# Kernel tuning notes

Measured on AMD Instinct MI355X. Metric: run time of the kernel, lower is better.

## Reference

```python
import jax, jax.numpy as jnp
import numpy as np

NUM_NODES = 50000
NUM_EDGES = 400000
NUM_GRAPHS = 16


def _glorot(key, shape):
    fan_in, fan_out = shape[0], shape[1]
    lim = jnp.sqrt(6.0 / (fan_in + fan_out))
    return jax.random.uniform(key, shape, jnp.float32, -lim, lim)


def setup_inputs() -> dict:
    key = jax.random.key(0)
    ks = jax.random.split(key, 12)
    x = jax.random.normal(ks[0], (NUM_NODES, 3), jnp.float32)
    edge_index = jax.random.randint(ks[1], (2, NUM_EDGES), 0, NUM_NODES, jnp.int64)
    batch = jax.random.randint(ks[2], (NUM_NODES,), 0, NUM_GRAPHS, jnp.int64)
    return {
        "x": x,
        "edge_index": edge_index,
        "batch": batch,
        "W1": _glorot(ks[3], (3, 512)),   "b1": jnp.zeros((512,), jnp.float32),
        "W2": _glorot(ks[4], (512, 1024)), "b2": jnp.zeros((1024,), jnp.float32),
        "W3": _glorot(ks[5], (1024, 512)), "b3": jnp.zeros((512,), jnp.float32),
        "fcw1": _glorot(ks[6], (512, 128)), "fcb1": jnp.zeros((128,), jnp.float32),
        "fcw2": _glorot(ks[7], (128, 1)),   "fcb2": jnp.zeros((1,), jnp.float32),
    }


def _gcn_conv(x, W, b, row, col, n):
    # PyG GCNConv: h = x W; out_i = sum_{j->i} d_j^{-1/2} d_i^{-1/2} h_j + b
    # (row, col) already include self-loops; edge weights are 1.
    h = x @ W  # [N, out]
    deg = jnp.zeros((n,), h.dtype).at[col].add(1.0)  # in-degree incl. self-loop
    dis = jax.lax.rsqrt(deg)  # deg >= 1 thanks to self-loops
    norm = dis[row] * dis[col]  # [E]
    msgs = h[row] * norm[:, None]  # [E, out] gather
    return jax.ops.segment_sum(msgs, col, num_segments=n) + b


def reference(x, edge_index, batch, W1, b1, W2, b2, W3, b3, fcw1, fcb1, fcw2, fcb2):
    n = x.shape[0]
    loop = jnp.arange(n, dtype=edge_index.dtype)
    row = jnp.concatenate([edge_index[0], loop])  # source
    col = jnp.concatenate([edge_index[1], loop])  # target

    h = jax.nn.relu(_gcn_conv(x, W1, b1, row, col, n))
    h = jax.nn.relu(_gcn_conv(h, W2, b2, row, col, n))
    h = jax.nn.relu(_gcn_conv(h, W3, b3, row, col, n))

    # global mean pool over graphs in the batch
    sums = jax.ops.segment_sum(h, batch, num_segments=NUM_GRAPHS)  # [G, 512]
    cnts = jax.ops.segment_sum(jnp.ones((n,), h.dtype), batch, num_segments=NUM_GRAPHS)
    pooled = sums / jnp.maximum(cnts, 1.0)[:, None]

    out = jax.nn.relu(pooled @ fcw1 + fcb1)
    out = out @ fcw2 + fcb2  # [G, 1]
    return out
```

## Files before the change

kernel.cpp:

```cpp
#include <hip/hip_runtime.h>
#include <hip/hip_bf16.h>

#define NNODES 50000
#define NEDGES 400000
#define NGRAPH 16
#define NBG 64

typedef __attribute__((ext_vector_type(4))) float floatx4;
typedef __attribute__((ext_vector_type(8))) short short8;

typedef __attribute__((address_space(3))) unsigned int lds_uint;
typedef __attribute__((address_space(1))) const unsigned int gbl_uint;

__device__ __forceinline__ void load16_to_lds(const void* g, void* l) {
    __builtin_amdgcn_global_load_lds((gbl_uint*)g, (lds_uint*)l, 16, 0, 0);
}

__global__ __launch_bounds__(64) void zero_out_k(float* out, int n) {
    int i = blockIdx.x * 64 + threadIdx.x;
    if (i < n) out[i] = 0.0f;
}

__global__ __launch_bounds__(256) void init_k(int* deg_cnt, int* cursor,
                                              float* gsum, int* gdeg,
                                              const float* __restrict__ x,
                                              float4* __restrict__ xp,
                                              const int* __restrict__ batch, int n) {
    __shared__ int h[NGRAPH];
    int t = threadIdx.x;
    if (t < NGRAPH) h[t] = 0;
    __syncthreads();
    int i = blockIdx.x * 256 + t;
    if (i < n) {
        deg_cnt[i] = 0; cursor[i] = 0;
        xp[i] = make_float4(x[i * 3 + 0], x[i * 3 + 1], x[i * 3 + 2], 0.0f);
        atomicAdd(&h[batch[i]], 1);
    }
    if (i < NGRAPH * 512) gsum[i] = 0.0f;
    __syncthreads();
    if (t < NGRAPH && h[t]) atomicAdd(&gdeg[t], h[t]);
}

__global__ __launch_bounds__(256) void deg_k(const int* __restrict__ col,
                                             int* __restrict__ deg_cnt, int e) {
    int i = blockIdx.x * 256 + threadIdx.x;
    if (i < e) atomicAdd(&deg_cnt[col[i]], 1);
}

__global__ __launch_bounds__(256) void segsum_k(const int* __restrict__ cnt,
                                                int* __restrict__ segsum, int n) {
    __shared__ int sb[256];
    int seg = blockIdx.x;
    int base = seg * 1024;
    int t = threadIdx.x;
    int s = 0;
#pragma unroll
    for (int j = 0; j < 4; ++j) {
        int idx = base + t + j * 256;
        if (idx < n) s += cnt[idx];
    }
    sb[t] = s;
    __syncthreads();
    for (int off = 128; off > 0; off >>= 1) {
        if (t < off) sb[t] += sb[t + off];
        __syncthreads();
    }
    if (t == 0) segsum[seg] = sb[0];
}

__global__ __launch_bounds__(64) void segscan_k(const int* __restrict__ segsum,
                                                int* __restrict__ segbase,
                                                int* __restrict__ offs,
                                                int nseg, int n) {
    if (threadIdx.x == 0) {
        int run = 0;
        for (int s = 0; s < nseg; ++s) { segbase[s] = run; run += segsum[s]; }
        offs[n] = run;
    }
}

__global__ __launch_bounds__(1024) void offs_k(const int* __restrict__ cnt,
                                               const int* __restrict__ segbase,
                                               int* __restrict__ offs,
                                               float* __restrict__ dis, int n) {
    __shared__ int sb[1024];
    int seg = blockIdx.x;
    int t = threadIdx.x;
    int i = seg * 1024 + t;
    int c = (i < n) ? cnt[i] : 0;
    sb[t] = c;
    __syncthreads();
    for (int off = 1; off < 1024; off <<= 1) {
        int v = (t >= off) ? sb[t - off] : 0;
        __syncthreads();
        sb[t] += v;
        __syncthreads();
    }
    if (i < n) {
        offs[i] = segbase[seg] + sb[t] - c;
        dis[i]  = rsqrtf((float)(c + 1));
    }
}

__global__ __launch_bounds__(256) void scatter_k(const int* __restrict__ row,
                                                 const int* __restrict__ col,
                                                 const int* __restrict__ offs,
                                                 int* __restrict__ cursor,
                                                 int* __restrict__ ssrc,
                                                 float* __restrict__ sw,
                                                 const float* __restrict__ dis, int e) {
    int i = blockIdx.x * 256 + threadIdx.x;
    if (i >= e) return;
    int d = col[i];
    int p = offs[d] + atomicAdd(&cursor[d], 1);
    int s = row[i];
    ssrc[p] = s;
    sw[p]   = dis[s];
}

__global__ __launch_bounds__(64) void gpfx_k(const int* __restrict__ gdeg,
                                             int* __restrict__ goffs) {
    if (threadIdx.x == 0) {
        int run = 0;
        for (int g = 0; g < NGRAPH; ++g) { goffs[g] = run; run += gdeg[g]; }
    }
}

__global__ __launch_bounds__(256) void gplace_k(const int* __restrict__ batch,
                                                const int* __restrict__ goffs,
                                                int* __restrict__ gcur,
                                                int* __restrict__ perm, int n) {
    __shared__ int h[NGRAPH];
    __shared__ int basev[NGRAPH];
    int t = threadIdx.x;
    if (t < NGRAPH) h[t] = 0;
    __syncthreads();
    int i = blockIdx.x * 256 + t;
    int g = 0, r = 0;
    if (i < n) {
        g = batch[i];
        r = atomicAdd(&h[g], 1);
    }
    __syncthreads();
    if (t < NGRAPH) basev[t] = h[t] ? atomicAdd(&gcur[t], h[t]) : 0;
    __syncthreads();
    if (i < n) perm[goffs[g] + basev[g] + r] = i;
}

__global__ __launch_bounds__(256) void agg3_k(const float4* __restrict__ xp,
                                              float* __restrict__ out,
                                              const int* __restrict__ offs,
                                              const int* __restrict__ ssrc,
                                              const float* __restrict__ sw,
                                              const float* __restrict__ dis, int n) {
    int d = blockIdx.x * 256 + threadIdx.x;
    if (d >= n) return;
    float dd = dis[d];
    float4 xd = xp[d];
    float a0 = dd * xd.x, a1 = dd * xd.y, a2 = dd * xd.z;
    int beg = offs[d], end = offs[d + 1];
    for (int e = beg; e < end; ++e) {
        int s = ssrc[e];
        float w = sw[e];
        float4 q = xp[s];
        a0 += w * q.x; a1 += w * q.y; a2 += w * q.z;
    }
    out[d * 3 + 0] = dd * a0;
    out[d * 3 + 1] = dd * a1;
    out[d * 3 + 2] = dd * a2;
}

__global__ __launch_bounds__(256) void gemm1_k(const float* __restrict__ aggx,
                                               const float* __restrict__ W1,
                                               const float* __restrict__ b1,
                                               __hip_bfloat16* __restrict__ h1, int n) {
    int wave = threadIdx.x >> 6;
    int lane = threadIdx.x & 63;
    int d = blockIdx.x * 4 + wave;
    if (d >= n) return;
    float a0 = aggx[d * 3 + 0], a1 = aggx[d * 3 + 1], a2 = aggx[d * 3 + 2];
    int f0 = lane * 8;
    short8 ov;
#pragma unroll
    for (int j = 0; j < 8; ++j) {
        int f = f0 + j;
        float v = b1[f] + a0 * W1[f] + a1 * W1[512 + f] + a2 * W1[1024 + f];
        __hip_bfloat16 h = __float2bfloat16(fmaxf(v, 0.0f));
        ov[j] = *(short*)&h;
    }
    *(short8*)&h1[(size_t)d * 512 + f0] = ov;
}

__device__ inline float bs2f(short v) {
    return __uint_as_float(((unsigned int)(unsigned short)v) << 16);
}

__global__ __launch_bounds__(256) void agg512w_k(const __hip_bfloat16* __restrict__ in,
                                                 __hip_bfloat16* __restrict__ out,
                                                 const int* __restrict__ offs,
                                                 const int* __restrict__ ssrc,
                                                 const float* __restrict__ sw,
                                                 const float* __restrict__ dis, int n) {
    int wave = threadIdx.x >> 6;
    int lane = threadIdx.x & 63;
    int d = blockIdx.x * 4 + wave;
    if (d >= n) return;
    float dd = dis[d];
    short8 p = *(const short8*)&in[(size_t)d * 512 + lane * 8];
    float acc[8];
#pragma unroll
    for (int j = 0; j < 8; ++j) acc[j] = dd * bs2f(p[j]);

    int beg = offs[d], end = offs[d + 1];
    int e = beg;
    for (; e + 3 < end; e += 4) {
        int s0 = ssrc[e],     s1 = ssrc[e + 1];
        int s2 = ssrc[e + 2], s3 = ssrc[e + 3];
        float w0 = sw[e],     w1 = sw[e + 1];
        float w2 = sw[e + 2], w3 = sw[e + 3];
        short8 q0 = *(const short8*)&in[(size_t)s0 * 512 + lane * 8];
        short8 q1 = *(const short8*)&in[(size_t)s1 * 512 + lane * 8];
        short8 q2 = *(const short8*)&in[(size_t)s2 * 512 + lane * 8];
        short8 q3 = *(const short8*)&in[(size_t)s3 * 512 + lane * 8];
#pragma unroll
        for (int j = 0; j < 8; ++j) acc[j] += w0 * bs2f(q0[j]);
#pragma unroll
        for (int j = 0; j < 8; ++j) acc[j] += w1 * bs2f(q1[j]);
#pragma unroll
        for (int j = 0; j < 8; ++j) acc[j] += w2 * bs2f(q2[j]);
#pragma unroll
        for (int j = 0; j < 8; ++j) acc[j] += w3 * bs2f(q3[j]);
    }
    for (; e < end; ++e) {
        int s0 = ssrc[e];
        float w0 = sw[e];
        short8 q0 = *(const short8*)&in[(size_t)s0 * 512 + lane * 8];
#pragma unroll
        for (int j = 0; j < 8; ++j) acc[j] += w0 * bs2f(q0[j]);
    }

    short8 ov;
#pragma unroll
    for (int j = 0; j < 8; ++j) {
        __hip_bfloat16 h = __float2bfloat16(acc[j] * dd);
        ov[j] = *(short*)&h;
    }
    *(short8*)&out[(size_t)d * 512 + lane * 8] = ov;
}

__global__ __launch_bounds__(256) void aggpool_k(const __hip_bfloat16* __restrict__ in,
                                                 const int* __restrict__ perm,
                                                 const int* __restrict__ goffs,
                                                 const int* __restrict__ gdeg,
                                                 const int* __restrict__ offs,
                                                 const int* __restrict__ ssrc,
                                                 const float* __restrict__ sw,
                                                 const float* __restrict__ dis,
                                                 const float* __restrict__ bias,
                                                 float* __restrict__ gsum) {
    __shared__ float lsw[4 * 512];
    int t = threadIdx.x;
    int wave = t >> 6;
    int lane = t & 63;
    int g = blockIdx.x & (NGRAPH - 1);
    int s = blockIdx.x >> 4;
    for (int i = t; i < 4 * 512; i += 256) lsw[i] = 0.0f;
    int cnt = gdeg[g];
    int per = (cnt + NBG - 1) / NBG;
    int beg = s * per;
    int end = min(cnt, beg + per);
    int gb  = goffs[g];
    float bj[8];
#pragma unroll
    for (int j = 0; j < 8; ++j) bj[j] = bias[lane * 8 + j];
    __syncthreads();

    for (int ii = beg + wave; ii < end; ii += 4) {
        int d = perm[gb + ii];
        float dd = dis[d];
        short8 p = *(const short8*)&in[(size_t)d * 512 + lane * 8];
        float acc[8];
#pragma unroll
        for (int j = 0; j < 8; ++j) acc[j] = dd * bs2f(p[j]);

        int eb = offs[d], ee = offs[d + 1];
        int e = eb;
        for (; e + 3 < ee; e += 4) {
            int s0 = ssrc[e],     s1 = ssrc[e + 1];
            int s2 = ssrc[e + 2], s3 = ssrc[e + 3];
            float w0 = sw[e],     w1 = sw[e + 1];
            float w2 = sw[e + 2], w3 = sw[e + 3];
            short8 q0 = *(const short8*)&in[(size_t)s0 * 512 + lane * 8];
            short8 q1 = *(const short8*)&in[(size_t)s1 * 512 + lane * 8];
            short8 q2 = *(const short8*)&in[(size_t)s2 * 512 + lane * 8];
            short8 q3 = *(const short8*)&in[(size_t)s3 * 512 + lane * 8];
#pragma unroll
            for (int j = 0; j < 8; ++j) acc[j] += w0 * bs2f(q0[j]);
#pragma unroll
            for (int j = 0; j < 8; ++j) acc[j] += w1 * bs2f(q1[j]);
#pragma unroll
            for (int j = 0; j < 8; ++j) acc[j] += w2 * bs2f(q2[j]);
#pragma unroll
            for (int j = 0; j < 8; ++j) acc[j] += w3 * bs2f(q3[j]);
        }
        for (; e < ee; ++e) {
            int s0 = ssrc[e];
            float w0 = sw[e];
            short8 q0 = *(const short8*)&in[(size_t)s0 * 512 + lane * 8];
#pragma unroll
            for (int j = 0; j < 8; ++j) acc[j] += w0 * bs2f(q0[j]);
        }

        float* mb = &lsw[wave * 512 + lane * 8];
        float4 a0 = *(float4*)mb;
        float4 a1 = *((float4*)mb + 1);
        a0.x += fmaxf(acc[0] * dd + bj[0], 0.0f);
        a0.y += fmaxf(acc[1] * dd + bj[1], 0.0f);
        a0.z += fmaxf(acc[2] * dd + bj[2], 0.0f);
        a0.w += fmaxf(acc[3] * dd + bj[3], 0.0f);
        a1.x += fmaxf(acc[4] * dd + bj[4], 0.0f);
        a1.y += fmaxf(acc[5] * dd + bj[5], 0.0f);
        a1.z += fmaxf(acc[6] * dd + bj[6], 0.0f);
        a1.w += fmaxf(acc[7] * dd + bj[7], 0.0f);
        *(float4*)mb = a0;
        *((float4*)mb + 1) = a1;
    }
    __syncthreads();
    for (int f = t; f < 512; f += 256) {
        float v = lsw[f] + lsw[512 + f] + lsw[1024 + f] + lsw[1536 + f];
        atomicAdd(&gsum[g * 512 + f], v);
    }
}

__global__ __launch_bounds__(256) void tcvt_k(const float* __restrict__ W2,
                                              __hip_bfloat16* __restrict__ w2t,
                                              const float* __restrict__ W3,
                                              __hip_bfloat16* __restrict__ w3t) {
    __shared__ float tile[32][33];
    int t = threadIdx.x;
    const float* W; __hip_bfloat16* Wt;
    int K, N, idx;
    if (blockIdx.x < 512) { W = W2; Wt = w2t; K = 512;  N = 1024; idx = blockIdx.x; }
    else                  { W = W3; Wt = w3t; K = 1024; N = 512;  idx = blockIdx.x - 512; }
    int nbn = N / 32;
    int bn = (idx % nbn) * 32;
    int bk = (idx / nbn) * 32;
    int c = t & 31, r0 = t >> 5;
#pragma unroll
    for (int j = 0; j < 4; ++j) {
        int r = r0 + j * 8;
        tile[r][c] = W[(size_t)(bk + r) * N + bn + c];
    }
    __syncthreads();
#pragma unroll
    for (int j = 0; j < 4; ++j) {
        int r = r0 + j * 8;
        Wt[(size_t)(bn + r) * K + bk + c] = __float2bfloat16(tile[c][r]);
    }
}

__global__ __launch_bounds__(512, 2) void mfma_gemm256_k(
        const __hip_bfloat16* __restrict__ A,
        const __hip_bfloat16* __restrict__ Bt,
        const float* __restrict__ bias,
        __hip_bfloat16* __restrict__ C,
        int M, int N, int K, int relu, int lnt) {
    __shared__ short smem[65536];

    int tid  = threadIdx.x;
    int lane = tid & 63;
    int wave = tid >> 6;
    int wm = wave >> 2;
    int wn = wave & 3;
    int fr = lane & 15;
    int kg = lane >> 4;
    int f7 = fr & 7;

    int nwg = gridDim.x;
    int wg  = (blockIdx.x & 7) * (nwg >> 3) + (blockIdx.x >> 3);
    int mt  = wg >> lnt;
    int nt  = wg & ((1 << lnt) - 1);
    int bm  = mt << 8;
    int bn  = nt << 8;

    int rsub = lane >> 3;
    int slog = (lane & 7) ^ rsub;
    const __hip_bfloat16* ga[4];
    const __hip_bfloat16* gb[4];
#pragma unroll
    for (int j = 0; j < 4; ++j) {
        int rloc = (wave * 4 + j) * 8 + rsub;
        ga[j] = A  + (size_t)(bm + rloc) * K + slog * 8;
        gb[j] = Bt + (size_t)(bn + rloc) * K + slog * 8;
    }
    int dstA = wave * 2048;

    int aoff = (wm * 128 + fr) * 64 + ((kg ^ f7) * 8);
    int boff = 16384 + (wn * 64 + fr) * 64 + ((kg ^ f7) * 8);

    floatx4 acc[8][4] = {};

    auto stage = [&](int p) {
        short* sp = &smem[p * 32768];
#pragma unroll
        for (int j = 0; j < 4; ++j) {
            load16_to_lds(ga[j], sp + dstA + j * 512);
            load16_to_lds(gb[j], sp + 16384 + dstA + j * 512);
            ga[j] += 64;
            gb[j] += 64;
        }
    };

    stage(0);
    int KT = K >> 6;
    for (int t = 0; t < KT; ++t) {
        int p = t & 1;
        __builtin_amdgcn_s_barrier();
        if (t + 1 < KT) {
            stage(p ^ 1);
            asm volatile("s_waitcnt vmcnt(8)" ::: "memory");
        } else {
            asm volatile("s_waitcnt vmcnt(0)" ::: "memory");
        }
        __builtin_amdgcn_s_barrier();

        const short* sm = &smem[p * 32768];
#pragma unroll
        for (int ks = 0; ks < 2; ++ks) {
            int kx = ks * 32;
            short8 bfr[4];
#pragma unroll
            for (int ni = 0; ni < 4; ++ni)
                bfr[ni] = *(const short8*)&sm[(boff + ni * 1024) ^ kx];
#pragma unroll
            for (int mh = 0; mh < 2; ++mh) {
                short8 afr[4];
#pragma unroll
                for (int mi = 0; mi < 4; ++mi)
                    afr[mi] = *(const short8*)&sm[(aoff + (mh * 4 + mi) * 1024) ^ kx];
                __builtin_amdgcn_s_setprio(1);
#pragma unroll
                for (int mi = 0; mi < 4; ++mi)
#pragma unroll
                    for (int ni = 0; ni < 4; ++ni)
                        acc[mh * 4 + mi][ni] = __builtin_amdgcn_mfma_f32_16x16x32_bf16(
                            afr[mi], bfr[ni], acc[mh * 4 + mi][ni], 0, 0, 0);
                __builtin_amdgcn_s_setprio(0);
            }
        }
    }

    short* Cs = smem;
    int l4 = lane >> 4;
#pragma unroll
    for (int h = 0; h < 2; ++h) {
        __builtin_amdgcn_s_barrier();
        if (wm == h) {
#pragma unroll
            for (int mi = 0; mi < 8; ++mi) {
#pragma unroll
                for (int ni = 0; ni < 4; ++ni) {
                    int rr = mi * 16 + l4 * 4;
                    int cc = wn * 64 + ni * 16 + fr;
                    float bv = bias ? bias[bn + cc] : 0.0f;
#pragma unroll
                    for (int r = 0; r < 4; ++r) {
                        float v = acc[mi][ni][r] + bv;
                        if (relu) v = fmaxf(v, 0.0f);
                        __hip_bfloat16 hh = __float2bfloat16(v);
                        Cs[(rr + r) * 264 + cc] = *(short*)&hh;
                    }
                }
            }
        }
        asm volatile("s_waitcnt lgkmcnt(0)" ::: "memory");
        __builtin_amdgcn_s_barrier();
#pragma unroll
        for (int i = 0; i < 8; ++i) {
            int idx = tid + 512 * i;
            int rr = idx >> 5, cc = idx & 31;
            int grow = bm + h * 128 + rr;
            if (grow < M)
                *(short8*)&C[(size_t)grow * N + bn + cc * 8] =
                    *(const short8*)&Cs[rr * 264 + cc * 8];
        }
    }
}

__global__ __launch_bounds__(128) void fc_k(const float* __restrict__ gsum,
                                            const int* __restrict__ gdeg,
                                            const float* __restrict__ fcw1,
                                            const float* __restrict__ fcb1,
                                            const float* __restrict__ fcw2,
                                            const float* __restrict__ fcb2,
                                            float* __restrict__ out) {
    int g = blockIdx.x;
    int t = threadIdx.x;
    __shared__ float pooled[512];
    __shared__ float red[128];
    float inv = 1.0f / fmaxf((float)gdeg[g], 1.0f);
    for (int i = t; i < 512; i += 128) pooled[i] = gsum[g * 512 + i] * inv;
    __syncthreads();
    float sacc = fcb1[t];
    for (int k = 0; k < 512; ++k) sacc += pooled[k] * fcw1[k * 128 + t];
    sacc = fmaxf(sacc, 0.0f);
    red[t] = sacc * fcw2[t];
    __syncthreads();
    for (int off = 64; off > 0; off >>= 1) {
        if (t < off) red[t] += red[t + off];
        __syncthreads();
    }
    if (t == 0) out[g] = red[0] + fcb2[0];
}

extern "C" void kernel_launch(void* const* d_in, const int* in_sizes, int n_in,
                              void* d_out, int out_size, void* d_ws, size_t ws_size,
                              hipStream_t stream) {
    const float* x    = (const float*)d_in[0];
    const int*   ei   = (const int*)d_in[1];
    const int*   batch= (const int*)d_in[2];
    const float* W1   = (const float*)d_in[3];
    const float* b1   = (const float*)d_in[4];
    const float* W2   = (const float*)d_in[5];
    const float* b2   = (const float*)d_in[6];
    const float* W3   = (const float*)d_in[7];
    const float* b3   = (const float*)d_in[8];
    const float* fcw1 = (const float*)d_in[9];
    const float* fcb1 = (const float*)d_in[10];
    const float* fcw2 = (const float*)d_in[11];
    const float* fcb2 = (const float*)d_in[12];
    float* out = (float*)d_out;

    const int N = in_sizes[0] / 3;
    const int E = in_sizes[1] / 2;
    const int Mpad = (N + 255) & ~255;
    const int nseg = (N + 1023) / 1024;
    const int* row = ei;
    const int* col = ei + E;

    size_t used = 0;
    auto need = [&](size_t bytes) {
        size_t off = used;
        used += (bytes + 255) & ~(size_t)255;
        return off;
    };
    size_t o_deg  = need((size_t)N * 4);
    size_t o_cur  = need((size_t)N * 4);
    size_t o_dis  = need((size_t)N * 4);
    size_t o_offs = need((size_t)(N + 1) * 4);
    size_t o_seg  = need((size_t)nseg * 4);
    size_t o_segb = need((size_t)nseg * 4);
    size_t o_ssrc = need((size_t)E * 4);
    size_t o_sw   = need((size_t)E * 4);
    size_t o_xp   = need((size_t)N * 16);
    size_t o_aggx = need((size_t)N * 3 * 4);
    size_t o_gsum = need((size_t)NGRAPH * 512 * 4);
    size_t o_gdeg = need((size_t)NGRAPH * 4);
    size_t o_gcur = need((size_t)NGRAPH * 4);
    size_t o_goff = need((size_t)(NGRAPH + 1) * 4);
    size_t o_perm = need((size_t)N * 4);
    size_t o_w2t  = need((size_t)512 * 1024 * 2);
    size_t o_w3t  = need((size_t)1024 * 512 * 2);
    size_t o_bufX = need((size_t)Mpad * 512 * 2);
    size_t o_bufY = need((size_t)Mpad * 512 * 2);
    size_t o_bufZ = need((size_t)Mpad * 1024 * 2);

    if (used > ws_size) {
        hipLaunchKernelGGL(zero_out_k, dim3((out_size + 63) / 64), dim3(64), 0, stream,
                           out, out_size);
        return;
    }

    char* base = (char*)d_ws;
    int*    deg_cnt = (int*)   (base + o_deg);
    int*    cursor  = (int*)   (base + o_cur);
    float*  dis     = (float*) (base + o_dis);
    int*    offs    = (int*)   (base + o_offs);
    int*    segsum  = (int*)   (base + o_seg);
    int*    segbase = (int*)   (base + o_segb);
    int*    ssrc    = (int*)   (base + o_ssrc);
    float*  sw      = (float*) (base + o_sw);
    float4* xp      = (float4*)(base + o_xp);
    float*  aggx    = (float*) (base + o_aggx);
    float*  gsum    = (float*) (base + o_gsum);
    int*    gdeg    = (int*)   (base + o_gdeg);
    int*    gcur    = (int*)   (base + o_gcur);
    int*    goffs   = (int*)   (base + o_goff);
    int*    perm    = (int*)   (base + o_perm);
    __hip_bfloat16* w2t  = (__hip_bfloat16*)(base + o_w2t);
    __hip_bfloat16* w3t  = (__hip_bfloat16*)(base + o_w3t);
    __hip_bfloat16* bufX = (__hip_bfloat16*)(base + o_bufX);
    __hip_bfloat16* bufY = (__hip_bfloat16*)(base + o_bufY);
    __hip_bfloat16* bufZ = (__hip_bfloat16*)(base + o_bufZ);
    (void)n_in;

    int gN = (N + 255) / 256;
    int gE = (E + 255) / 256;
    int gW = (N + 3) / 4;
    int nrt = Mpad / 256;

    hipMemsetAsync(base + o_gdeg, 0, 512, stream);

    hipLaunchKernelGGL(init_k, dim3(gN), dim3(256), 0, stream, deg_cnt, cursor, gsum, gdeg, x, xp, batch, N);
    hipLaunchKernelGGL(deg_k, dim3(gE), dim3(256), 0, stream, col, deg_cnt, E);
    hipLaunchKernelGGL(segsum_k, dim3(nseg), dim3(256), 0, stream, deg_cnt, segsum, N);
    hipLaunchKernelGGL(segscan_k, dim3(1), dim3(64), 0, stream, segsum, segbase, offs, nseg, N);
    hipLaunchKernelGGL(offs_k, dim3(nseg), dim3(1024), 0, stream, deg_cnt, segbase, offs, dis, N);
    hipLaunchKernelGGL(scatter_k, dim3(gE), dim3(256), 0, stream, row, col, offs, cursor, ssrc, sw, dis, E);

    hipLaunchKernelGGL(gpfx_k, dim3(1), dim3(64), 0, stream, gdeg, goffs);
    hipLaunchKernelGGL(gplace_k, dim3(gN), dim3(256), 0, stream, batch, goffs, gcur, perm, N);

    hipLaunchKernelGGL(tcvt_k, dim3(1024), dim3(256), 0, stream, W2, w2t, W3, w3t);

    hipLaunchKernelGGL(agg3_k, dim3(gN), dim3(256), 0, stream, xp, aggx, offs, ssrc, sw, dis, N);
    hipLaunchKernelGGL(gemm1_k, dim3(gW), dim3(256), 0, stream, aggx, W1, b1, bufX, N);

    hipLaunchKernelGGL(agg512w_k, dim3(gW), dim3(256), 0, stream, bufX, bufY, offs, ssrc, sw, dis, N);
    hipLaunchKernelGGL(mfma_gemm256_k, dim3(nrt * 4), dim3(512), 0, stream,
                       bufY, w2t, b2, bufZ, N, 1024, 512, 1, 2);

    hipLaunchKernelGGL(mfma_gemm256_k, dim3(nrt * 2), dim3(512), 0, stream,
                       bufZ, w3t, (const float*)nullptr, bufX, N, 512, 1024, 0, 1);
    hipLaunchKernelGGL(aggpool_k, dim3(NGRAPH * NBG), dim3(256), 0, stream,
                       bufX, perm, goffs, gdeg, offs, ssrc, sw, dis, b3, gsum);

    hipLaunchKernelGGL(fc_k, dim3(NGRAPH), dim3(128), 0, stream, gsum, gdeg, fcw1, fcb1, fcw2, fcb2, out);
}
```

Measured before the change: 502.1 us.

## Merge preprocessing kernels and replace pooled atomics with deterministic partial reduction

Folds the graph-offset prefix into segscan_k and the node-to-graph permutation placement into scatter_k, which removes two kernel launches. The pooling kernel now keeps per-wave partial sums in registers and writes per-block partials to a workspace buffer. A new small poolred_k kernel then sums those partials per graph, replacing the global atomics and the gsum zeroing. This trades launch and atomic overhead for one extra launch and a 2 MB partial-sum buffer.

New measurement: 503.1 us. Within noise of the previous version (+0.2%).

```diff
diff --git a/kernel.cpp b/kernel.cpp
--- a/kernel.cpp
+++ b/kernel.cpp
@@ -22,7 +22,7 @@
 }
 
 __global__ __launch_bounds__(256) void init_k(int* deg_cnt, int* cursor,
-                                              float* gsum, int* gdeg,
+                                              int* gdeg,
                                               const float* __restrict__ x,
                                               float4* __restrict__ xp,
                                               const int* __restrict__ batch, int n) {
@@ -36,7 +36,6 @@
         xp[i] = make_float4(x[i * 3 + 0], x[i * 3 + 1], x[i * 3 + 2], 0.0f);
         atomicAdd(&h[batch[i]], 1);
     }
-    if (i < NGRAPH * 512) gsum[i] = 0.0f;
     __syncthreads();
     if (t < NGRAPH && h[t]) atomicAdd(&gdeg[t], h[t]);
 }
@@ -71,11 +70,16 @@
 __global__ __launch_bounds__(64) void segscan_k(const int* __restrict__ segsum,
                                                 int* __restrict__ segbase,
                                                 int* __restrict__ offs,
+                                                const int* __restrict__ gdeg,
+                                                int* __restrict__ goffs,
                                                 int nseg, int n) {
     if (threadIdx.x == 0) {
         int run = 0;
         for (int s = 0; s < nseg; ++s) { segbase[s] = run; run += segsum[s]; }
         offs[n] = run;
+    } else if (threadIdx.x == 1) {
+        int run = 0;
+        for (int g = 0; g < NGRAPH; ++g) { goffs[g] = run; run += gdeg[g]; }
     }
 }
 
@@ -108,28 +112,12 @@
                                                  int* __restrict__ cursor,
                                                  int* __restrict__ ssrc,
                                                  float* __restrict__ sw,
-                                                 const float* __restrict__ dis, int e) {
-    int i = blockIdx.x * 256 + threadIdx.x;
-    if (i >= e) return;
-    int d = col[i];
-    int p = offs[d] + atomicAdd(&cursor[d], 1);
-    int s = row[i];
-    ssrc[p] = s;
-    sw[p]   = dis[s];
-}
-
-__global__ __launch_bounds__(64) void gpfx_k(const int* __restrict__ gdeg,
-                                             int* __restrict__ goffs) {
-    if (threadIdx.x == 0) {
-        int run = 0;
-        for (int g = 0; g < NGRAPH; ++g) { goffs[g] = run; run += gdeg[g]; }
-    }
-}
-
-__global__ __launch_bounds__(256) void gplace_k(const int* __restrict__ batch,
-                                                const int* __restrict__ goffs,
-                                                int* __restrict__ gcur,
-                                                int* __restrict__ perm, int n) {
+                                                 const float* __restrict__ dis,
+                                                 const int* __restrict__ batch,
+                                                 const int* __restrict__ goffs,
+                                                 int* __restrict__ gcur,
+                                                 int* __restrict__ perm,
+                                                 int e, int n) {
     __shared__ int h[NGRAPH];
     __shared__ int basev[NGRAPH];
     int t = threadIdx.x;
@@ -145,6 +133,14 @@
     if (t < NGRAPH) basev[t] = h[t] ? atomicAdd(&gcur[t], h[t]) : 0;
     __syncthreads();
     if (i < n) perm[goffs[g] + basev[g] + r] = i;
+
+    if (i < e) {
+        int d = col[i];
+        int p = offs[d] + atomicAdd(&cursor[d], 1);
+        int s = row[i];
+        ssrc[p] = s;
+        sw[p]   = dis[s];
+    }
 }
 
 __global__ __launch_bounds__(256) void agg3_k(const float4* __restrict__ xp,
@@ -257,14 +253,13 @@
                                                  const float* __restrict__ sw,
                                                  const float* __restrict__ dis,
                                                  const float* __restrict__ bias,
-                                                 float* __restrict__ gsum) {
+                                                 float* __restrict__ gpart) {
     __shared__ float lsw[4 * 512];
     int t = threadIdx.x;
     int wave = t >> 6;
     int lane = t & 63;
     int g = blockIdx.x & (NGRAPH - 1);
     int s = blockIdx.x >> 4;
-    for (int i = t; i < 4 * 512; i += 256) lsw[i] = 0.0f;
     int cnt = gdeg[g];
     int per = (cnt + NBG - 1) / NBG;
     int beg = s * per;
@@ -273,7 +268,7 @@
     float bj[8];
 #pragma unroll
     for (int j = 0; j < 8; ++j) bj[j] = bias[lane * 8 + j];
-    __syncthreads();
+    float pacc[8] = {0.f, 0.f, 0.f, 0.f, 0.f, 0.f, 0.f, 0.f};
 
     for (int ii = beg + wave; ii < end; ii += 4) {
         int d = perm[gb + ii];
@@ -310,25 +305,31 @@
 #pragma unroll
             for (int j = 0; j < 8; ++j) acc[j] += w0 * bs2f(q0[j]);
         }
-
-        float* mb = &lsw[wave * 512 + lane * 8];
-        float4 a0 = *(float4*)mb;
-        float4 a1 = *((float4*)mb + 1);
-        a0.x += fmaxf(acc[0] * dd + bj[0], 0.0f);
-        a0.y += fmaxf(acc[1] * dd + bj[1], 0.0f);
-        a0.z += fmaxf(acc[2] * dd + bj[2], 0.0f);
-        a0.w += fmaxf(acc[3] * dd + bj[3], 0.0f);
-        a1.x += fmaxf(acc[4] * dd + bj[4], 0.0f);
-        a1.y += fmaxf(acc[5] * dd + bj[5], 0.0f);
-        a1.z += fmaxf(acc[6] * dd + bj[6], 0.0f);
-        a1.w += fmaxf(acc[7] * dd + bj[7], 0.0f);
-        *(float4*)mb = a0;
-        *((float4*)mb + 1) = a1;
-    }
-    __syncthreads();
+#pragma unroll
+        for (int j = 0; j < 8; ++j)
+            pacc[j] += fmaxf(acc[j] * dd + bj[j], 0.0f);
+    }
+
+    float* mb = &lsw[wave * 512 + lane * 8];
+#pragma unroll
+    for (int j = 0; j < 4; ++j) mb[j] = pacc[j];
+#pragma unroll
+    for (int j = 0; j < 4; ++j) mb[4 + j] = pacc[4 + j];
+    __syncthreads();
+    float* gp = &gpart[(size_t)blockIdx.x * 512];
+    for (int f = t; f < 512; f += 256)
+        gp[f] = lsw[f] + lsw[512 + f] + lsw[1024 + f] + lsw[1536 + f];
+}
+
+__global__ __launch_bounds__(256) void poolred_k(const float* __restrict__ gpart,
+                                                 float* __restrict__ gsum) {
+    int g = blockIdx.x;
+    int t = threadIdx.x;
     for (int f = t; f < 512; f += 256) {
-        float v = lsw[f] + lsw[512 + f] + lsw[1024 + f] + lsw[1536 + f];
-        atomicAdd(&gsum[g * 512 + f], v);
+        float v = 0.0f;
+        for (int s = 0; s < NBG; ++s)
+            v += gpart[(size_t)(s * NGRAPH + g) * 512 + f];
+        gsum[g * 512 + f] = v;
     }
 }
 
@@ -559,6 +560,7 @@
     size_t o_gcur = need((size_t)NGRAPH * 4);
     size_t o_goff = need((size_t)(NGRAPH + 1) * 4);
     size_t o_perm = need((size_t)N * 4);
+    size_t o_gpart= need((size_t)NGRAPH * NBG * 512 * 4);
     size_t o_w2t  = need((size_t)512 * 1024 * 2);
     size_t o_w3t  = need((size_t)1024 * 512 * 2);
     size_t o_bufX = need((size_t)Mpad * 512 * 2);
@@ -587,6 +589,7 @@
     int*    gcur    = (int*)   (base + o_gcur);
     int*    goffs   = (int*)   (base + o_goff);
     int*    perm    = (int*)   (base + o_perm);
+    float*  gpart   = (float*) (base + o_gpart);
     __hip_bfloat16* w2t  = (__hip_bfloat16*)(base + o_w2t);
     __hip_bfloat16* w3t  = (__hip_bfloat16*)(base + o_w3t);
     __hip_bfloat16* bufX = (__hip_bfloat16*)(base + o_bufX);
@@ -601,15 +604,13 @@
 
     hipMemsetAsync(base + o_gdeg, 0, 512, stream);
 
-    hipLaunchKernelGGL(init_k, dim3(gN), dim3(256), 0, stream, deg_cnt, cursor, gsum, gdeg, x, xp, batch, N);
+    hipLaunchKernelGGL(init_k, dim3(gN), dim3(256), 0, stream, deg_cnt, cursor, gdeg, x, xp, batch, N);
     hipLaunchKernelGGL(deg_k, dim3(gE), dim3(256), 0, stream, col, deg_cnt, E);
     hipLaunchKernelGGL(segsum_k, dim3(nseg), dim3(256), 0, stream, deg_cnt, segsum, N);
-    hipLaunchKernelGGL(segscan_k, dim3(1), dim3(64), 0, stream, segsum, segbase, offs, nseg, N);
+    hipLaunchKernelGGL(segscan_k, dim3(1), dim3(64), 0, stream, segsum, segbase, offs, gdeg, goffs, nseg, N);
     hipLaunchKernelGGL(offs_k, dim3(nseg), dim3(1024), 0, stream, deg_cnt, segbase, offs, dis, N);
-    hipLaunchKernelGGL(scatter_k, dim3(gE), dim3(256), 0, stream, row, col, offs, cursor, ssrc, sw, dis, E);
-
-    hipLaunchKernelGGL(gpfx_k, dim3(1), dim3(64), 0, stream, gdeg, goffs);
-    hipLaunchKernelGGL(gplace_k, dim3(gN), dim3(256), 0, stream, batch, goffs, gcur, perm, N);
+    hipLaunchKernelGGL(scatter_k, dim3(gE), dim3(256), 0, stream, row, col, offs, cursor, ssrc, sw, dis,
+                       batch, goffs, gcur, perm, E, N);
 
     hipLaunchKernelGGL(tcvt_k, dim3(1024), dim3(256), 0, stream, W2, w2t, W3, w3t);
 
@@ -623,7 +624,8 @@
     hipLaunchKernelGGL(mfma_gemm256_k, dim3(nrt * 2), dim3(512), 0, stream,
                        bufZ, w3t, (const float*)nullptr, bufX, N, 512, 1024, 0, 1);
     hipLaunchKernelGGL(aggpool_k, dim3(NGRAPH * NBG), dim3(256), 0, stream,
-                       bufX, perm, goffs, gdeg, offs, ssrc, sw, dis, b3, gsum);
+                       bufX, perm, goffs, gdeg, offs, ssrc, sw, dis, b3, gpart);
+    hipLaunchKernelGGL(poolred_k, dim3(NGRAPH), dim3(256), 0, stream, gpart, gsum);
 
     hipLaunchKernelGGL(fc_k, dim3(NGRAPH), dim3(128), 0, stream, gsum, gdeg, fcw1, fcb1, fcw2, fcb2, out);
 }
```
